# Performance work log

Hardware: AMD Instinct MI355X
Metric: run time of the kernel (lower is better)

## Reference

```python
import jax, jax.numpy as jnp
import numpy as np

B, N, D_IN, D_MEM, LAYERS = 8, 2048, 128, 128, 3


def setup_inputs() -> dict:
    key = jax.random.key(0)
    k1, k2, k3, k4 = jax.random.split(key, 4)
    inputs = jax.random.normal(k1, (B, N, D_IN), dtype=jnp.float32)
    # attention-derived adjacency: nonnegative weights
    out_adj = jax.random.uniform(k2, (B, N, N), dtype=jnp.float32)
    # per-layer Linear weights (all layers 128->128 here, stacked) with
    # torch nn.Linear-style init scale 1/sqrt(fan_in)
    scale = 1.0 / np.sqrt(D_IN)
    W = jax.random.uniform(k3, (LAYERS, D_IN, D_MEM), minval=-scale, maxval=scale, dtype=jnp.float32)
    b = jax.random.uniform(k4, (LAYERS, D_MEM), minval=-scale, maxval=scale, dtype=jnp.float32)
    return {"inputs": inputs, "out_adj": out_adj, "W": W, "b": b}


def reference(inputs, out_adj, W, b):
    # GCN.forward (eval mode; dropout = identity)
    adj = out_adj  # [B, N, N]
    denom = jnp.sum(adj, axis=2, keepdims=True) + 1.0  # [B, N, 1]
    outputs = inputs  # [B, N, D]
    for l in range(W.shape[0]):
        Ax = jnp.einsum('bij,bjd->bid', adj, outputs)      # aggregate
        AxW = Ax @ W[l] + b[l]                             # per-layer linear
        outputs = jax.nn.relu(AxW / denom)                 # normalize + activate
    return outputs
```

## Files before the change

kernel.cpp:

```cpp
#include <hip/hip_runtime.h>

#define NN 2048
#define DD 128

typedef _Float16 f16x8 __attribute__((ext_vector_type(8)));
typedef float f32x4 __attribute__((ext_vector_type(4)));


__global__ __launch_bounds__(256) void prep_kernel(
    const float* __restrict__ W, _Float16* __restrict__ Wt) {
  int idx = blockIdx.x * 256 + threadIdx.x;
  int l = idx >> 14, r = idx & 16383, d = r >> 7, k = r & 127;
  Wt[idx] = (_Float16)W[l * 16384 + k * 128 + d];
}

__global__ __launch_bounds__(256) void prepAll_kernel(
    const float* __restrict__ adj, _Float16* __restrict__ adjH,
    float* __restrict__ rdg, const float* __restrict__ X,
    _Float16* __restrict__ Xt) {
  __shared__ float rs[16][4];
  const int bx = blockIdx.x, tid = threadIdx.x;
  const int lane = tid & 63, wave = tid >> 6;
  const int quad = lane >> 4, l15 = lane & 15;

  if (bx < 1024) {
    const int it = bx & 127, batch = bx >> 7;
    const float* Ap = adj + ((size_t)(batch * NN) + it * 16 + l15) * NN + quad * 8;
    _Float16* Hp = adjH + (size_t)batch * NN * NN + ((size_t)it * 64) * 512 + lane * 8;
    float s = 0.f;
#pragma unroll
    for (int j = 0; j < 16; ++j) {
      const int ct = wave + 4 * j;
      float4 a0 = *(const float4*)(Ap + ct * 32);
      float4 a1 = *(const float4*)(Ap + ct * 32 + 4);
      s += ((a0.x + a0.y) + (a0.z + a0.w)) + ((a1.x + a1.y) + (a1.z + a1.w));
      f16x8 h = {(_Float16)a0.x, (_Float16)a0.y, (_Float16)a0.z, (_Float16)a0.w,
                 (_Float16)a1.x, (_Float16)a1.y, (_Float16)a1.z, (_Float16)a1.w};
      *(f16x8*)(Hp + (size_t)ct * 512) = h;
    }
    s += __shfl_xor(s, 16);
    s += __shfl_xor(s, 32);
    if (lane < 16) rs[lane][wave] = s;
    __syncthreads();
    if (tid < 16) {
      float t = rs[tid][0] + rs[tid][1] + rs[tid][2] + rs[tid][3];
      rdg[batch * NN + it * 16 + tid] = 1.0f / (t + 1.0f);
    }
  } else if (bx < 1536) {
    const int vbx = bx - 1024;
    const int batch = vbx & 7, nt = vbx >> 3;
    const size_t batA = (size_t)batch * (128 * NN);
#pragma unroll
    for (int dtl = 0; dtl < 2; ++dtl) {
      const int dt = wave * 2 + dtl;
      const float* Xp = X + ((size_t)(batch * NN) + nt * 32 + quad * 8) * DD + dt * 16 + l15;
      f16x8 v;
#pragma unroll
      for (int e = 0; e < 8; ++e) v[e] = (_Float16)Xp[(size_t)e * DD];
      *(f16x8*)(Xt + batA + ((size_t)(dt * 64 + nt)) * 512 + lane * 8) = v;
    }
  }
}

__device__ __forceinline__ void epiGemm(const float (*Xs)[132],
    const _Float16* __restrict__ Wf, int d0, int quad, int l15,
    f32x4 (&o)[2][2]) {
#pragma unroll
  for (int kk = 0; kk < 128; kk += 32) {
    f16x8 a0 = *(const f16x8*)(Wf + (d0 + l15) * DD + kk + quad * 8);
    f16x8 a1 = *(const f16x8*)(Wf + (d0 + 16 + l15) * DD + kk + quad * 8);
#pragma unroll
    for (int fi = 0; fi < 2; ++fi) {
      const float* xp = &Xs[fi * 16 + l15][kk + quad * 8];
      f16x8 b = {(_Float16)xp[0], (_Float16)xp[1], (_Float16)xp[2], (_Float16)xp[3],
                 (_Float16)xp[4], (_Float16)xp[5], (_Float16)xp[6], (_Float16)xp[7]};
      o[0][fi] = __builtin_amdgcn_mfma_f32_16x16x32_f16(a0, b, o[0][fi], 0, 0, 0);
      o[1][fi] = __builtin_amdgcn_mfma_f32_16x16x32_f16(a1, b, o[1][fi], 0, 0, 0);
    }
  }
}

template<int MODE>
__global__ __launch_bounds__(256) void aggL_kernel(
    const _Float16* __restrict__ adjH, const float* __restrict__ rdg,
    const _Float16* __restrict__ At, const float* __restrict__ bias,
    const _Float16* __restrict__ WA, const _Float16* __restrict__ WB,
    _Float16* __restrict__ Yout, float* __restrict__ out) {
  __shared__ _Float16 Bs[2][1024];
  __shared__ float Xs[32][132];
  __shared__ float bsh[128];
  __shared__ float rdsh[32];

  const int tid = threadIdx.x, bx = blockIdx.x;
  const int batch = bx & 7, iblk = bx >> 3, i0 = iblk * 32;
  const int lane = tid & 63, wave = tid >> 6;
  const int quad = lane >> 4, l15 = lane & 15, d0 = wave * 32;

  const size_t batA = (size_t)batch * (128 * NN);
  const size_t batB = (size_t)batch * ((size_t)NN * NN);
  const _Float16* Ap0 = At + batA + ((size_t)(2 * wave) * 64) * 512 + lane * 8;
  const _Float16* Ap1 = At + batA + ((size_t)(2 * wave + 1) * 64) * 512 + lane * 8;
  const _Float16* BpW = adjH + batB + ((size_t)(iblk * 2 + wave) * 64) * 512 + lane * 8;

  if (tid < 128) bsh[tid] = bias[tid];
  if (tid < 32) rdsh[tid] = rdg[batch * NN + i0 + tid];

  if (wave < 2) {
    f16x8 h0 = *(const f16x8*)(BpW);
    *(f16x8*)&Bs[0][wave * 512 + lane * 8] = h0;
  }
  f16x8 aC0 = *(const f16x8*)(Ap0);
  f16x8 aC1 = *(const f16x8*)(Ap1);
  f32x4 acc[2][2] = {};
  __syncthreads();

#define STEP(ct, CB, NB)                                                                   \
  {                                                                                        \
    const bool stg = (wave < 2) && ((ct) < 63);                                            \
    f16x8 hN = {};                                                                         \
    if (stg) hN = *(const f16x8*)(BpW + ((ct) + 1) * 512);                                 \
    const int ctn = ((ct) < 63) ? (ct) + 1 : (ct);                                         \
    f16x8 aN0 = *(const f16x8*)(Ap0 + ctn * 512);                                          \
    f16x8 aN1 = *(const f16x8*)(Ap1 + ctn * 512);                                          \
    f16x8 b0 = *(const f16x8*)&Bs[CB][lane * 8];                                           \
    f16x8 b1 = *(const f16x8*)&Bs[CB][512 + lane * 8];                                     \
    acc[0][0] = __builtin_amdgcn_mfma_f32_16x16x32_f16(aC0, b0, acc[0][0], 0, 0, 0);       \
    acc[0][1] = __builtin_amdgcn_mfma_f32_16x16x32_f16(aC0, b1, acc[0][1], 0, 0, 0);       \
    acc[1][0] = __builtin_amdgcn_mfma_f32_16x16x32_f16(aC1, b0, acc[1][0], 0, 0, 0);       \
    acc[1][1] = __builtin_amdgcn_mfma_f32_16x16x32_f16(aC1, b1, acc[1][1], 0, 0, 0);       \
    if (stg) *(f16x8*)&Bs[NB][wave * 512 + lane * 8] = hN;                                 \
    __syncthreads();                                                                       \
    aC0 = aN0;                                                                             \
    aC1 = aN1;                                                                             \
  }

  for (int ct = 0; ct < 64; ct += 2) {
    STEP(ct, 0, 1)
    STEP(ct + 1, 1, 0)
  }
#undef STEP

  const float rv0 = rdsh[l15], rv1 = rdsh[16 + l15];
  f32x4 accY[2][2];

  if (MODE == 0) {
#pragma unroll
    for (int df = 0; df < 2; ++df)
#pragma unroll
      for (int fi = 0; fi < 2; ++fi)
#pragma unroll
        for (int r = 0; r < 4; ++r)
          Xs[fi * 16 + l15][d0 + df * 16 + quad * 4 + r] = acc[df][fi][r];
    __syncthreads();
    f32x4 acc2[2][2] = {};
    epiGemm(Xs, WA, d0, quad, l15, acc2);
    __syncthreads();
#pragma unroll
    for (int df = 0; df < 2; ++df)
#pragma unroll
      for (int fi = 0; fi < 2; ++fi)
#pragma unroll
        for (int r = 0; r < 4; ++r) {
          int d = d0 + df * 16 + quad * 4 + r;
          float rv = fi ? rv1 : rv0;
          Xs[fi * 16 + l15][d] = fmaxf((acc2[df][fi][r] + bsh[d]) * rv, 0.f);
        }
    __syncthreads();
    f32x4 acc3[2][2] = {};
    epiGemm(Xs, WB, d0, quad, l15, acc3);
#pragma unroll
    for (int df = 0; df < 2; ++df)
#pragma unroll
      for (int fi = 0; fi < 2; ++fi) accY[df][fi] = acc3[df][fi];
  } else {
#pragma unroll
    for (int df = 0; df < 2; ++df)
#pragma unroll
      for (int fi = 0; fi < 2; ++fi)
#pragma unroll
        for (int r = 0; r < 4; ++r) {
          int d = d0 + df * 16 + quad * 4 + r;
          float rv = fi ? rv1 : rv0;
          Xs[fi * 16 + l15][d] = fmaxf((acc[df][fi][r] + bsh[d]) * rv, 0.f);
        }
    __syncthreads();
    if (MODE == 2) {
      float* outB = out + (size_t)(batch * NN + i0) * DD;
#pragma unroll
      for (int u = 0; u < 4; ++u) {
        int c = tid + 256 * u;
        int i = c >> 5, f4 = (c & 31) * 4;
        *(float4*)(outB + (size_t)i * DD + f4) = *(const float4*)&Xs[i][f4];
      }
      return;
    }
    f32x4 acc2[2][2] = {};
    epiGemm(Xs, WA, d0, quad, l15, acc2);
#pragma unroll
    for (int df = 0; df < 2; ++df)
#pragma unroll
      for (int fi = 0; fi < 2; ++fi) accY[df][fi] = acc2[df][fi];
  }

  __syncthreads();
  _Float16* Yst = (_Float16*)Xs;
#pragma unroll
  for (int df = 0; df < 2; ++df)
#pragma unroll
    for (int fi = 0; fi < 2; ++fi)
#pragma unroll
      for (int r = 0; r < 4; ++r)
        Yst[(d0 + df * 16 + quad * 4 + r) * 40 + fi * 16 + l15] =
            (_Float16)accY[df][fi][r];
  __syncthreads();
  const int nt = i0 >> 5;
  _Float16* Yb = Yout + batA;
#pragma unroll
  for (int dtl = 0; dtl < 2; ++dtl) {
    const int dt = 2 * wave + dtl;
    f16x8 v = *(const f16x8*)(&Yst[(dt * 16 + l15) * 40 + quad * 8]);
    *(f16x8*)(Yb + ((size_t)(dt * 64 + nt)) * 512 + lane * 8) = v;
  }
}

__global__ __launch_bounds__(256) void gemmY_kernel(
    const float* __restrict__ X, const _Float16* __restrict__ Wt,
    _Float16* __restrict__ Yt) {
  const int bx = blockIdx.x;
  const int batch = bx & 7, n0 = (bx >> 3) * 32;
  const int tid = threadIdx.x, lane = tid & 63, wave = tid >> 6;
  const int quad = lane >> 4, l15 = lane & 15, d0 = wave * 32;
  const float* Xb = X + (size_t)(batch * NN + n0) * DD;
  f32x4 acc[2][2] = {};
#pragma unroll
  for (int kk = 0; kk < 128; kk += 32) {
    f16x8 a0 = *(const f16x8*)(Wt + (d0 + l15) * DD + kk + quad * 8);
    f16x8 a1 = *(const f16x8*)(Wt + (d0 + 16 + l15) * DD + kk + quad * 8);
#pragma unroll
    for (int fi = 0; fi < 2; ++fi) {
      const float* xp = Xb + (size_t)(fi * 16 + l15) * DD + kk + quad * 8;
      float4 x0 = *(const float4*)xp;
      float4 x1 = *(const float4*)(xp + 4);
      f16x8 b = {(_Float16)x0.x, (_Float16)x0.y, (_Float16)x0.z, (_Float16)x0.w,
                 (_Float16)x1.x, (_Float16)x1.y, (_Float16)x1.z, (_Float16)x1.w};
      acc[0][fi] = __builtin_amdgcn_mfma_f32_16x16x32_f16(a0, b, acc[0][fi], 0, 0, 0);
      acc[1][fi] = __builtin_amdgcn_mfma_f32_16x16x32_f16(a1, b, acc[1][fi], 0, 0, 0);
    }
  }
  _Float16* YtB = Yt + (size_t)batch * DD * NN;
#pragma unroll
  for (int df = 0; df < 2; ++df)
#pragma unroll
    for (int fi = 0; fi < 2; ++fi)
#pragma unroll
      for (int r = 0; r < 4; ++r)
        YtB[(size_t)(d0 + df * 16 + quad * 4 + r) * NN + n0 + fi * 16 + l15] =
            (_Float16)acc[df][fi][r];
}

template<bool LAST>
__global__ __launch_bounds__(256) void agg_kernel(
    const float* __restrict__ adj, const _Float16* __restrict__ Yt,
    const float* __restrict__ bias, const _Float16* __restrict__ Wn,
    _Float16* __restrict__ Ytn, float* __restrict__ out) {
  __shared__ _Float16 Bsl[2][32 * 64];
  __shared__ float Xs[32][132];
  __shared__ float bsh[128];
  __shared__ float rd[32];

  const int tid = threadIdx.x, bx = blockIdx.x;
  const int batch = bx & 7, i0 = (bx >> 3) * 32;
  const int lane = tid & 63, wave = tid >> 6;
  const int quad = lane >> 4, l15 = lane & 15, d0 = wave * 32;
  const int ai = tid >> 3, ac = tid & 7;
  const int sc = ac ^ (ai & 7);

  const float* adjR = adj + (size_t)(batch * NN + i0 + ai) * NN + ac * 8;
  const _Float16* YtB = Yt + (size_t)batch * DD * NN;
  const _Float16* Ya0 = YtB + (size_t)(d0 + l15) * NN;
  const _Float16* Ya1 = YtB + (size_t)(d0 + 16 + l15) * NN;

  if (tid < 128) bsh[tid] = bias[tid];

  f32x4 acc[2][2] = {};
  float rowsum = 0.f;

  float4 av0 = *(const float4*)(adjR);
  float4 av1 = *(const float4*)(adjR + 4);
  f16x8 a[2][2];
#pragma unroll
  for (int k2 = 0; k2 < 2; ++k2) {
    a[k2][0] = *(const f16x8*)(Ya0 + k2 * 32 + quad * 8);
    a[k2][1] = *(const f16x8*)(Ya1 + k2 * 32 + quad * 8);
  }

  for (int ko = 0; ko < 32; ++ko) {
    rowsum += ((av0.x + av0.y) + (av0.z + av0.w)) + ((av1.x + av1.y) + (av1.z + av1.w));
    f16x8 h = {(_Float16)av0.x, (_Float16)av0.y, (_Float16)av0.z, (_Float16)av0.w,
               (_Float16)av1.x, (_Float16)av1.y, (_Float16)av1.z, (_Float16)av1.w};
    *(f16x8*)(&Bsl[ko & 1][ai * 64 + sc * 8]) = h;
    f16x8 an[2][2];
    if (ko < 31) {
      const int kb = (ko + 1) * 64;
      av0 = *(const float4*)(adjR + kb);
      av1 = *(const float4*)(adjR + kb + 4);
#pragma unroll
      for (int k2 = 0; k2 < 2; ++k2) {
        an[k2][0] = *(const f16x8*)(Ya0 + kb + k2 * 32 + quad * 8);
        an[k2][1] = *(const f16x8*)(Ya1 + kb + k2 * 32 + quad * 8);
      }
    }
    __syncthreads();
    const _Float16* B = Bsl[ko & 1];
#pragma unroll
    for (int k2 = 0; k2 < 2; ++k2)
#pragma unroll
      for (int fi = 0; fi < 2; ++fi) {
        const int row = fi * 16 + l15;
        const int ch = (k2 * 4 + quad) ^ (row & 7);
        f16x8 b = *(const f16x8*)(&B[row * 64 + ch * 8]);
        acc[0][fi] = __builtin_amdgcn_mfma_f32_16x16x32_f16(a[k2][0], b, acc[0][fi], 0, 0, 0);
        acc[1][fi] = __builtin_amdgcn_mfma_f32_16x16x32_f16(a[k2][1], b, acc[1][fi], 0, 0, 0);
      }
#pragma unroll
    for (int k2 = 0; k2 < 2; ++k2) { a[k2][0] = an[k2][0]; a[k2][1] = an[k2][1]; }
  }

  rowsum += __shfl_xor(rowsum, 1);
  rowsum += __shfl_xor(rowsum, 2);
  rowsum += __shfl_xor(rowsum, 4);
  if (ac == 0) rd[ai] = 1.0f / (rowsum + 1.0f);
  __syncthreads();

#pragma unroll
  for (int df = 0; df < 2; ++df)
#pragma unroll
    for (int fi = 0; fi < 2; ++fi)
#pragma unroll
      for (int r = 0; r < 4; ++r) {
        int d = d0 + df * 16 + quad * 4 + r;
        int i = fi * 16 + l15;
        Xs[i][d] = fmaxf((acc[df][fi][r] + bsh[d]) * rd[i], 0.f);
      }
  __syncthreads();

  if (LAST) {
    float* outB = out + (size_t)(batch * NN + i0) * DD;
#pragma unroll
    for (int u = 0; u < 4; ++u) {
      int c = tid + 256 * u;
      int i = c >> 5, f4 = (c & 31) * 4;
      *(float4*)(outB + (size_t)i * DD + f4) = *(const float4*)&Xs[i][f4];
    }
  } else {
    f32x4 acc2[2][2] = {};
    epiGemm(Xs, Wn, d0, quad, l15, acc2);
    _Float16* YnB = Ytn + (size_t)batch * DD * NN;
#pragma unroll
    for (int df = 0; df < 2; ++df)
#pragma unroll
      for (int fi = 0; fi < 2; ++fi)
#pragma unroll
        for (int r = 0; r < 4; ++r)
          YnB[(size_t)(d0 + df * 16 + quad * 4 + r) * NN + i0 + fi * 16 + l15] =
              (_Float16)acc2[df][fi][r];
  }
}

extern "C" void kernel_launch(void* const* d_in, const int* in_sizes, int n_in,
                              void* d_out, int out_size, void* d_ws, size_t ws_size,
                              hipStream_t stream) {
  const float* x0   = (const float*)d_in[0];
  const float* adj  = (const float*)d_in[1];
  const float* W    = (const float*)d_in[2];
  const float* bias = (const float*)d_in[3];
  float* out = (float*)d_out;

  _Float16* Wt   = (_Float16*)d_ws;
  float*    rdg  = (float*)((char*)d_ws + (1u << 17));
  _Float16* Xt   = (_Float16*)((char*)d_ws + (1u << 20));
  _Float16* Y1t  = (_Float16*)((char*)d_ws + (5u << 20));
  _Float16* Y2t  = (_Float16*)((char*)d_ws + (9u << 20));
  _Float16* adjH = (_Float16*)((char*)d_ws + (16u << 20));

  const bool big = ws_size >= (81ull << 20);

  dim3 blk(256);
  prep_kernel<<<192, blk, 0, stream>>>(W, Wt);
  if (big) {
    prepAll_kernel<<<1536, blk, 0, stream>>>(adj, adjH, rdg, x0, Xt);
    aggL_kernel<0><<<512, blk, 0, stream>>>(adjH, rdg, Xt, bias, Wt, Wt + 16384, Y1t, nullptr);
    aggL_kernel<1><<<512, blk, 0, stream>>>(adjH, rdg, Y1t, bias + 128, Wt + 32768, nullptr, Y2t, nullptr);
    aggL_kernel<2><<<512, blk, 0, stream>>>(adjH, rdg, Y2t, bias + 256, nullptr, nullptr, nullptr, out);
  } else {
    _Float16* YtA  = Xt;
    _Float16* YtB_ = (_Float16*)d_out;
    gemmY_kernel<<<512, blk, 0, stream>>>(x0, Wt, YtA);
    agg_kernel<false><<<512, blk, 0, stream>>>(adj, YtA,  bias,       Wt + 16384, YtB_, nullptr);
    agg_kernel<false><<<512, blk, 0, stream>>>(adj, YtB_, bias + 128, Wt + 32768, YtA,  nullptr);
    agg_kernel<true ><<<512, blk, 0, stream>>>(adj, YtA,  bias + 256, nullptr,    nullptr, out);
  }
}
```

Baseline: 294.4 us.

## Replace LDS double-buffered adjacency staging with deep register prefetch pipeline

The aggregation kernel no longer stages adjacency tiles through shared memory with a barrier each step. Every wave now loads both adjacency fragments straight from global memory into registers, using an 8-deep prefetch ring for both operands. This removes 64 per-step __syncthreads and the LDS round trip, so more loads stay in flight. In exchange each wave loads the adjacency itself (4x redundant global/L2 reads), and the ring raises register pressure, which may reduce occupancy.

```diff
diff --git a/kernel.cpp b/kernel.cpp
--- a/kernel.cpp
+++ b/kernel.cpp
@@ -80,13 +80,14 @@
   }
 }
 
+#define PD 8
+
 template<int MODE>
-__global__ __launch_bounds__(256) void aggL_kernel(
+__global__ __launch_bounds__(256) void aggP_kernel(
     const _Float16* __restrict__ adjH, const float* __restrict__ rdg,
     const _Float16* __restrict__ At, const float* __restrict__ bias,
     const _Float16* __restrict__ WA, const _Float16* __restrict__ WB,
     _Float16* __restrict__ Yout, float* __restrict__ out) {
-  __shared__ _Float16 Bs[2][1024];
   __shared__ float Xs[32][132];
   __shared__ float bsh[128];
   __shared__ float rdsh[32];
@@ -98,48 +99,42 @@
 
   const size_t batA = (size_t)batch * (128 * NN);
   const size_t batB = (size_t)batch * ((size_t)NN * NN);
+  const int it0 = iblk * 2;
   const _Float16* Ap0 = At + batA + ((size_t)(2 * wave) * 64) * 512 + lane * 8;
   const _Float16* Ap1 = At + batA + ((size_t)(2 * wave + 1) * 64) * 512 + lane * 8;
-  const _Float16* BpW = adjH + batB + ((size_t)(iblk * 2 + wave) * 64) * 512 + lane * 8;
+  const _Float16* Bp0 = adjH + batB + ((size_t)it0 * 64) * 512 + lane * 8;
+  const _Float16* Bp1 = adjH + batB + ((size_t)(it0 + 1) * 64) * 512 + lane * 8;
 
   if (tid < 128) bsh[tid] = bias[tid];
   if (tid < 32) rdsh[tid] = rdg[batch * NN + i0 + tid];
 
-  if (wave < 2) {
-    f16x8 h0 = *(const f16x8*)(BpW);
-    *(f16x8*)&Bs[0][wave * 512 + lane * 8] = h0;
-  }
-  f16x8 aC0 = *(const f16x8*)(Ap0);
-  f16x8 aC1 = *(const f16x8*)(Ap1);
   f32x4 acc[2][2] = {};
-  __syncthreads();
-
-#define STEP(ct, CB, NB)                                                                   \
-  {                                                                                        \
-    const bool stg = (wave < 2) && ((ct) < 63);                                            \
-    f16x8 hN = {};                                                                         \
-    if (stg) hN = *(const f16x8*)(BpW + ((ct) + 1) * 512);                                 \
-    const int ctn = ((ct) < 63) ? (ct) + 1 : (ct);                                         \
-    f16x8 aN0 = *(const f16x8*)(Ap0 + ctn * 512);                                          \
-    f16x8 aN1 = *(const f16x8*)(Ap1 + ctn * 512);                                          \
-    f16x8 b0 = *(const f16x8*)&Bs[CB][lane * 8];                                           \
-    f16x8 b1 = *(const f16x8*)&Bs[CB][512 + lane * 8];                                     \
-    acc[0][0] = __builtin_amdgcn_mfma_f32_16x16x32_f16(aC0, b0, acc[0][0], 0, 0, 0);       \
-    acc[0][1] = __builtin_amdgcn_mfma_f32_16x16x32_f16(aC0, b1, acc[0][1], 0, 0, 0);       \
-    acc[1][0] = __builtin_amdgcn_mfma_f32_16x16x32_f16(aC1, b0, acc[1][0], 0, 0, 0);       \
-    acc[1][1] = __builtin_amdgcn_mfma_f32_16x16x32_f16(aC1, b1, acc[1][1], 0, 0, 0);       \
-    if (stg) *(f16x8*)&Bs[NB][wave * 512 + lane * 8] = hN;                                 \
-    __syncthreads();                                                                       \
-    aC0 = aN0;                                                                             \
-    aC1 = aN1;                                                                             \
-  }
-
-  for (int ct = 0; ct < 64; ct += 2) {
-    STEP(ct, 0, 1)
-    STEP(ct + 1, 1, 0)
-  }
-#undef STEP
-
+  f16x8 qa0[PD], qa1[PD], qb0[PD], qb1[PD];
+
+#define PF(j)                                              \
+  { const int s_ = (j) & (PD - 1);                         \
+    qa0[s_] = *(const f16x8*)(Ap0 + (size_t)(j) * 512);    \
+    qa1[s_] = *(const f16x8*)(Ap1 + (size_t)(j) * 512);    \
+    qb0[s_] = *(const f16x8*)(Bp0 + (size_t)(j) * 512);    \
+    qb1[s_] = *(const f16x8*)(Bp1 + (size_t)(j) * 512); }
+#define MM(j)                                                                                   \
+  { const int s_ = (j) & (PD - 1);                                                              \
+    acc[0][0] = __builtin_amdgcn_mfma_f32_16x16x32_f16(qa0[s_], qb0[s_], acc[0][0], 0, 0, 0);   \
+    acc[0][1] = __builtin_amdgcn_mfma_f32_16x16x32_f16(qa0[s_], qb1[s_], acc[0][1], 0, 0, 0);   \
+    acc[1][0] = __builtin_amdgcn_mfma_f32_16x16x32_f16(qa1[s_], qb0[s_], acc[1][0], 0, 0, 0);   \
+    acc[1][1] = __builtin_amdgcn_mfma_f32_16x16x32_f16(qa1[s_], qb1[s_], acc[1][1], 0, 0, 0); }
+
+#pragma unroll
+  for (int j = 0; j < PD; ++j) PF(j)
+#pragma unroll
+  for (int ct = 0; ct < 64; ++ct) {
+    MM(ct)
+    if (ct + PD < 64) PF(ct + PD)
+  }
+#undef PF
+#undef MM
+
+  __syncthreads();
   const float rv0 = rdsh[l15], rv1 = rdsh[16 + l15];
   f32x4 accY[2][2];
 
@@ -389,9 +384,9 @@
   prep_kernel<<<192, blk, 0, stream>>>(W, Wt);
   if (big) {
     prepAll_kernel<<<1536, blk, 0, stream>>>(adj, adjH, rdg, x0, Xt);
-    aggL_kernel<0><<<512, blk, 0, stream>>>(adjH, rdg, Xt, bias, Wt, Wt + 16384, Y1t, nullptr);
-    aggL_kernel<1><<<512, blk, 0, stream>>>(adjH, rdg, Y1t, bias + 128, Wt + 32768, nullptr, Y2t, nullptr);
-    aggL_kernel<2><<<512, blk, 0, stream>>>(adjH, rdg, Y2t, bias + 256, nullptr, nullptr, nullptr, out);
+    aggP_kernel<0><<<512, blk, 0, stream>>>(adjH, rdg, Xt, bias, Wt, Wt + 16384, Y1t, nullptr);
+    aggP_kernel<1><<<512, blk, 0, stream>>>(adjH, rdg, Y1t, bias + 128, Wt + 32768, nullptr, Y2t, nullptr);
+    aggP_kernel<2><<<512, blk, 0, stream>>>(adjH, rdg, Y2t, bias + 256, nullptr, nullptr, nullptr, out);
   } else {
     _Float16* YtA  = Xt;
     _Float16* YtB_ = (_Float16*)d_out;
```

Result: no change. 290.6 us (-1.3%).
